# Performance work log

Hardware: AMD Instinct MI355X
Metric: run time of the kernel (lower is better)

The kernel has to match this reference:

```python
import jax, jax.numpy as jnp
import numpy as np

D_MODEL = 256
LAMBDA_DECAY = 0.5
NEG_INF = -1e9


def setup_inputs() -> dict:
    key = jax.random.key(0)
    k0, k1, k2, k3 = jax.random.split(key, 4)
    B, S = 8, 2048
    inputs = jax.random.normal(k0, (B, S, 2), dtype=jnp.float32)
    # Dense(d_model, use_bias=False) on a scalar feature -> weight [1, d_model]
    Wq = jax.random.normal(k1, (1, D_MODEL), dtype=jnp.float32) * 0.05
    Wk = jax.random.normal(k2, (1, D_MODEL), dtype=jnp.float32) * 0.05
    Wv = jax.random.normal(k3, (1, D_MODEL), dtype=jnp.float32) * 0.05
    return {"inputs": inputs, "Wq": Wq, "Wk": Wk, "Wv": Wv}


def reference(inputs, Wq, Wk, Wv):
    sizes = inputs[:, :, 0]    # [B, S]
    heights = inputs[:, :, 1]  # [B, S]
    h = heights[:, :, None]    # [B, S, 1]
    q = h * Wq[0]              # [B, S, d] (scalar-feature dense)
    k = h * Wk[0]
    v = h * Wv[0]
    dk = jnp.asarray(q.shape[-1], dtype=q.dtype)
    logits = jnp.einsum('bsd,btd->bst', q, k) / jnp.sqrt(dk)  # [B, S, S]
    # additive distance penalty from pairwise |size_i - size_j|
    penalty = -LAMBDA_DECAY * jnp.abs(sizes[:, :, None] - sizes[:, None, :])
    logits = logits + penalty
    # mask branch: valid where heights != 0
    attn_mask = (heights != 0).astype(logits.dtype)  # [B, S]
    key_mask = attn_mask[:, None, :]                 # [B, 1, S]
    query_mask = attn_mask[:, :, None]               # [B, S, 1]
    logits = logits + (1.0 - key_mask) * NEG_INF
    logits = logits + (1.0 - query_mask) * NEG_INF
    weights = jax.nn.softmax(logits, axis=-1)
    weights = weights * key_mask
    out = jnp.einsum('bst,btd->bsd', weights, v)  # [B, S, d]
    return out
```

## Files before the change

kernel.cpp:

```cpp
#include <hip/hip_runtime.h>

#define SEQ 2048
#define DM  256
#define WAVES 4
#define THREADS (WAVES * 64)
#define RPW 4
#define ROWS_PER_BLOCK (WAVES * RPW)

__global__ __launch_bounds__(THREADS) void dwsa_kernel(
    const float* __restrict__ in,
    const float* __restrict__ Wq,
    const float* __restrict__ Wk,
    const float* __restrict__ Wv,
    float* __restrict__ out)
{
    __shared__ float4 sv4[SEQ / 2];

    const int tid  = threadIdx.x;
    const int lane = tid & 63;
    const int wave = tid >> 6;

    const float HALF_L2E = 0.72134752f;

    const int blocks_per_b = SEQ / ROWS_PER_BLOCK;
    const int b  = blockIdx.x / blocks_per_b;
    const int s0 = (blockIdx.x % blocks_per_b) * ROWS_PER_BLOCK;

    const float4* inb4 = (const float4*)(in + (size_t)b * SEQ * 2);
    #pragma unroll
    for (int t = tid; t < SEQ / 2; t += THREADS) {
        float4 p = inb4[t];
        p.x = (p.y == 0.0f) ? 7.2e8f : HALF_L2E * p.x;
        p.z = (p.w == 0.0f) ? 7.2e8f : HALF_L2E * p.z;
        sv4[t] = p;
    }

    float cpart = 0.0f;
    #pragma unroll
    for (int j = 0; j < 4; ++j) {
        const int i = lane + 64 * j;
        cpart = fmaf(Wq[i], Wk[i], cpart);
    }
    #pragma unroll
    for (int off = 32; off; off >>= 1) cpart += __shfl_xor(cpart, off);
    const float c_l2e = cpart * (1.0f / 16.0f) * 1.44269504f;

    const float4 wv = ((const float4*)Wv)[lane];

    __syncthreads();

    const int rbase = s0 + wave * RPW;
    float ssr[RPW], chs[RPW], se[RPW], seh[RPW];
    #pragma unroll
    for (int r = 0; r < RPW; ++r) {
        const float2 me = ((const float2*)sv4)[rbase + r];
        ssr[r] = me.x;
        chs[r] = c_l2e * me.y;
        se[r] = 0.0f; seh[r] = 0.0f;
    }

    #pragma unroll
    for (int i = 0; i < SEQ / 128; ++i) {
        const float4 kt = sv4[lane + 64 * i];
        #pragma unroll
        for (int r = 0; r < RPW; ++r) {
            {
                const float dl = ssr[r] - kt.x;
                const float e  = __builtin_amdgcn_exp2f(fmaf(chs[r], kt.y, -fabsf(dl)));
                se[r] += e;
                seh[r] = fmaf(e, kt.y, seh[r]);
            }
            {
                const float dl = ssr[r] - kt.z;
                const float e  = __builtin_amdgcn_exp2f(fmaf(chs[r], kt.w, -fabsf(dl)));
                se[r] += e;
                seh[r] = fmaf(e, kt.w, seh[r]);
            }
        }
    }

    #pragma unroll
    for (int r = 0; r < RPW; ++r) {
        float a = se[r], h = seh[r];
        #pragma unroll
        for (int off = 32; off; off >>= 1) {
            a += __shfl_xor(a, off);
            h += __shfl_xor(h, off);
        }
        a = (a == 0.0f) ? 1.0f : a;
        const float A = h / a;
        float4 o;
        o.x = A * wv.x; o.y = A * wv.y; o.z = A * wv.z; o.w = A * wv.w;
        ((float4*)(out + ((size_t)b * SEQ + rbase + r) * DM))[lane] = o;
    }
}

extern "C" void kernel_launch(void* const* d_in, const int* in_sizes, int n_in,
                              void* d_out, int out_size, void* d_ws, size_t ws_size,
                              hipStream_t stream) {
    const float* in = (const float*)d_in[0];
    const float* Wq = (const float*)d_in[1];
    const float* Wk = (const float*)d_in[2];
    const float* Wv = (const float*)d_in[3];
    float* out = (float*)d_out;

    const int B = in_sizes[0] / (SEQ * 2);
    dim3 grid(B * (SEQ / ROWS_PER_BLOCK));
    dwsa_kernel<<<grid, THREADS, 0, stream>>>(in, Wq, Wk, Wv, out);
}
```

Before: 15.69 us.

## Double rows per wave, pack accumulators as float2, use nontemporal output stores

Rows per wave go from 4 to 8, so each LDS key load is reused across more query rows and the grid shrinks to 512 blocks. The per-row sum and weighted-sum accumulators become two-wide vectors, which lets the compiler emit packed FP32 add and fma instructions. Output writes switch to nontemporal stores to avoid polluting the cache. In exchange, the halved block count may underfill the GPU, and register pressure rises.

After: 15.89 us. About the same (+1.3%).

```diff
diff --git a/kernel.cpp b/kernel.cpp
--- a/kernel.cpp
+++ b/kernel.cpp
@@ -4,8 +4,11 @@
 #define DM  256
 #define WAVES 4
 #define THREADS (WAVES * 64)
-#define RPW 4
+#define RPW 8
 #define ROWS_PER_BLOCK (WAVES * RPW)
+
+typedef float f2 __attribute__((ext_vector_type(2)));
+typedef float f4 __attribute__((ext_vector_type(4)));
 
 __global__ __launch_bounds__(THREADS) void dwsa_kernel(
     const float* __restrict__ in,
@@ -45,43 +48,42 @@
     for (int off = 32; off; off >>= 1) cpart += __shfl_xor(cpart, off);
     const float c_l2e = cpart * (1.0f / 16.0f) * 1.44269504f;
 
-    const float4 wv = ((const float4*)Wv)[lane];
+    const f4 wv = ((const f4*)Wv)[lane];
 
     __syncthreads();
 
     const int rbase = s0 + wave * RPW;
-    float ssr[RPW], chs[RPW], se[RPW], seh[RPW];
+    float ssr[RPW], chs[RPW];
+    f2 se2[RPW], seh2[RPW];
     #pragma unroll
     for (int r = 0; r < RPW; ++r) {
         const float2 me = ((const float2*)sv4)[rbase + r];
         ssr[r] = me.x;
         chs[r] = c_l2e * me.y;
-        se[r] = 0.0f; seh[r] = 0.0f;
+        se2[r] = (f2){0.0f, 0.0f};
+        seh2[r] = (f2){0.0f, 0.0f};
     }
 
     #pragma unroll
     for (int i = 0; i < SEQ / 128; ++i) {
         const float4 kt = sv4[lane + 64 * i];
+        const f2 h2 = {kt.y, kt.w};
         #pragma unroll
         for (int r = 0; r < RPW; ++r) {
-            {
-                const float dl = ssr[r] - kt.x;
-                const float e  = __builtin_amdgcn_exp2f(fmaf(chs[r], kt.y, -fabsf(dl)));
-                se[r] += e;
-                seh[r] = fmaf(e, kt.y, seh[r]);
-            }
-            {
-                const float dl = ssr[r] - kt.z;
-                const float e  = __builtin_amdgcn_exp2f(fmaf(chs[r], kt.w, -fabsf(dl)));
-                se[r] += e;
-                seh[r] = fmaf(e, kt.w, seh[r]);
-            }
+            const float l0 = fmaf(chs[r], kt.y, -fabsf(ssr[r] - kt.x));
+            const float l1 = fmaf(chs[r], kt.w, -fabsf(ssr[r] - kt.z));
+            f2 e2;
+            e2.x = __builtin_amdgcn_exp2f(l0);
+            e2.y = __builtin_amdgcn_exp2f(l1);
+            se2[r]  += e2;
+            seh2[r] += e2 * h2;
         }
     }
 
     #pragma unroll
     for (int r = 0; r < RPW; ++r) {
-        float a = se[r], h = seh[r];
+        float a = se2[r].x + se2[r].y;
+        float h = seh2[r].x + seh2[r].y;
         #pragma unroll
         for (int off = 32; off; off >>= 1) {
             a += __shfl_xor(a, off);
@@ -89,9 +91,9 @@
         }
         a = (a == 0.0f) ? 1.0f : a;
         const float A = h / a;
-        float4 o;
-        o.x = A * wv.x; o.y = A * wv.y; o.z = A * wv.z; o.w = A * wv.w;
-        ((float4*)(out + ((size_t)b * SEQ + rbase + r) * DM))[lane] = o;
+        const f4 o = A * wv;
+        __builtin_nontemporal_store(
+            o, (f4*)(out + ((size_t)b * SEQ + rbase + r) * DM) + lane);
     }
 }
 
```
